# Kernel tuning notes

Hardware: AMD Instinct MI355X
Metric: run time of the kernel (lower is better)

The kernel has to match this reference:

```python
import jax, jax.numpy as jnp
import numpy as np
import math

NUM_HEADS = 16
D_MODEL = 1024
D_HEAD = D_MODEL // NUM_HEADS
B, S = 2, 2048


def setup_inputs() -> dict:
    key = jax.random.key(0)
    k1, k2 = jax.random.split(key)
    query = jax.random.normal(k1, (B, S, D_MODEL), dtype=jnp.float32)
    # causal mask: True where masked (j > i)
    mask = jnp.broadcast_to(jnp.triu(jnp.ones((S, S), dtype=bool), k=1), (B, S, S))
    W_o = jax.random.normal(k2, (D_MODEL, D_MODEL), dtype=jnp.float32) * (1.0 / math.sqrt(D_MODEL))
    b_o = jnp.zeros((D_MODEL,), dtype=jnp.float32)
    return {"query": query, "mask": mask, "W_o": W_o, "b_o": b_o}


def reference(query, mask, W_o, b_o):
    # NOTE: faithful to source — q/k/v linear layers are never applied in forward.
    # Self-attention: key = value = query.
    Bq, Sq, D = query.shape
    # split heads: [B, S, D] -> [B, H, S, dh]
    q = query.reshape(Bq, Sq, NUM_HEADS, D_HEAD).transpose(0, 2, 1, 3)
    k = q
    v = q
    # logits: [B, H, Sq, Sk]
    logits = jnp.einsum("bhqd,bhkd->bhqk", q, k) / math.sqrt(D_HEAD)
    logits = jnp.where(mask[:, None, :, :], -jnp.inf, logits)
    attn = jax.nn.softmax(logits, axis=-1)          # [B, H, Sq, Sk]
    out = jnp.einsum("bhqk,bhkd->bhqd", attn, v)    # [B, H, Sq, dh]
    # merge heads: [B, Sq, D]
    out = out.transpose(0, 2, 1, 3).reshape(Bq, Sq, D)
    # output projection (torch Linear: x @ W.T + b)
    return out @ W_o.T + b_o
```

## Files before the change

kernel.cpp:

```cpp
#include <hip/hip_runtime.h>
#include <hip/hip_bf16.h>
#include <stdint.h>

#define SEQ 2048
#define DMODEL 1024
#define NQT 16

typedef __attribute__((ext_vector_type(8))) short short8;
typedef __attribute__((ext_vector_type(4))) float floatx4;

__device__ __forceinline__ floatx4 mfma16x16x32(short8 a, short8 b, floatx4 c) {
  return __builtin_amdgcn_mfma_f32_16x16x32_bf16(a, b, c, 0, 0, 0);
}

__device__ __forceinline__ uint16_t f2bf(float x) {
  __hip_bfloat16 h = __float2bfloat16(x);
  return *reinterpret_cast<uint16_t*>(&h);
}

__device__ __forceinline__ void glds16(const uint16_t* g, uint16_t* l) {
  __builtin_amdgcn_global_load_lds(
      (const __attribute__((address_space(1))) uint32_t*)g,
      (__attribute__((address_space(3))) uint32_t*)(uint32_t)(uintptr_t)l,
      16, 0, 0);
}

__global__ __launch_bounds__(256) void cvt_kernel(
    const float* __restrict__ src, uint16_t* __restrict__ dst, int n4) {
  int i = blockIdx.x * 256 + threadIdx.x;
  if (i < n4) {
    float4 v = ((const float4*)src)[i];
    ushort4 r;
    r.x = f2bf(v.x); r.y = f2bf(v.y); r.z = f2bf(v.z); r.w = f2bf(v.w);
    ((ushort4*)dst)[i] = r;
  }
}

__device__ __forceinline__ int vt_idx(int d, int key) {
  return d * 64 + ((((key >> 3) ^ (d >> 3)) & 7) << 3) + (key & 7);
}

#define LDPP 72

__global__ __launch_bounds__(256, 2) void attn_kernel(
    const uint16_t* __restrict__ qbf, uint16_t* __restrict__ xout) {
  const int qt   = (NQT - 1) - (blockIdx.x >> 5);
  const int bh   = blockIdx.x & 31;
  const int b    = bh >> 4;
  const int h    = bh & 15;
  const int tid  = threadIdx.x;
  const int wave = tid >> 6;
  const int lane = tid & 63;
  const int l15  = lane & 15;
  const int quad = lane >> 4;

  __shared__ uint16_t Kp[2][2 * 2048];
  __shared__ uint16_t Vt[2][64 * 64];
  __shared__ uint16_t Ps[4][32 * LDPP];

  const uint16_t* kbase = qbf + (size_t)b * SEQ * DMODEL + h * 64;

  short8 qf[2][2];
  #pragma unroll
  for (int s = 0; s < 2; ++s)
    #pragma unroll
    for (int ks = 0; ks < 2; ++ks)
      qf[s][ks] = *(const short8*)(kbase +
          (size_t)(qt * 128 + s * 64 + wave * 16 + l15) * DMODEL + ks * 32 + quad * 8);

  floatx4 o_acc[2][4];
  float l_run[2][4];
  #pragma unroll
  for (int s = 0; s < 2; ++s) {
    #pragma unroll
    for (int dt = 0; dt < 4; ++dt) o_acc[s][dt] = (floatx4){0.f, 0.f, 0.f, 0.f};
    #pragma unroll
    for (int r = 0; r < 4; ++r) l_run[s][r] = 0.f;
  }

  const int r0 = tid >> 3;
  const int cg = (tid & 7) * 8;
  const int gkey = wave * 16 + (lane >> 2);
  const int gkp  = (lane & 3) * 8;

  auto stage = [&](int kt, int buf) {
    uint4 v0 = *(const uint4*)(kbase + (size_t)(kt * 64 + r0) * DMODEL + cg);
    uint4 v1 = *(const uint4*)(kbase + (size_t)(kt * 64 + 32 + r0) * DMODEL + cg);
    glds16(kbase + (size_t)(kt * 64 + gkey) * DMODEL + gkp,
           &Kp[buf][0 * 2048 + wave * 512 + lane * 8]);
    glds16(kbase + (size_t)(kt * 64 + gkey) * DMODEL + 32 + gkp,
           &Kp[buf][1 * 2048 + wave * 512 + lane * 8]);
    uint16_t t0[8], t1[8];
    *(uint4*)t0 = v0;
    *(uint4*)t1 = v1;
    #pragma unroll
    for (int i = 0; i < 8; ++i) Vt[buf][vt_idx(cg + i, r0)] = t0[i];
    #pragma unroll
    for (int i = 0; i < 8; ++i) Vt[buf][vt_idx(cg + i, 32 + r0)] = t1[i];
  };

  const int ktmax = 2 * qt + 1;
  stage(0, 0);

  for (int kt = 0; kt <= ktmax; ++kt) {
    __syncthreads();
    if (kt < ktmax) stage(kt + 1, (kt + 1) & 1);
    const int buf = kt & 1;

    #pragma unroll
    for (int s = 0; s < 2; ++s) {
      if (kt > 2 * qt + s) continue;
      const bool diag = (kt == 2 * qt + s);

      floatx4 sacc[4];
      #pragma unroll
      for (int nt = 0; nt < 4; ++nt) sacc[nt] = (floatx4){0.f, 0.f, 0.f, 0.f};
      #pragma unroll
      for (int ks = 0; ks < 2; ++ks)
        #pragma unroll
        for (int nt = 0; nt < 4; ++nt) {
          short8 kf = *(const short8*)&Kp[buf][ks * 2048 + (nt * 16 + l15) * 32 + quad * 8];
          sacc[nt] = mfma16x16x32(qf[s][ks], kf, sacc[nt]);
        }

      uint16_t* Pw = &Ps[wave][s * 16 * LDPP];
      #pragma unroll
      for (int nt = 0; nt < 4; ++nt) {
        const int lcol = nt * 16 + l15;
        #pragma unroll
        for (int r = 0; r < 4; ++r) {
          float p = __builtin_amdgcn_exp2f(fmaf(sacc[nt][r], 0.1803369f, -10.f));
          if (diag && lcol > wave * 16 + quad * 4 + r) p = 0.f;
          l_run[s][r] += p;
          Pw[(quad * 4 + r) * LDPP + lcol] = f2bf(p);
        }
      }

      #pragma unroll
      for (int ks = 0; ks < 2; ++ks) {
        short8 pf = *(const short8*)&Pw[l15 * LDPP + ks * 32 + quad * 8];
        #pragma unroll
        for (int dt = 0; dt < 4; ++dt) {
          short8 vf = *(const short8*)&Vt[buf][vt_idx(dt * 16 + l15, ks * 32 + quad * 8)];
          o_acc[s][dt] = mfma16x16x32(pf, vf, o_acc[s][dt]);
        }
      }
    }
  }

  #pragma unroll
  for (int s = 0; s < 2; ++s)
    #pragma unroll
    for (int r = 0; r < 4; ++r) {
      float l = l_run[s][r];
      #pragma unroll
      for (int off = 1; off < 16; off <<= 1) l += __shfl_xor(l, off, 64);
      float inv = 1.0f / l;
      int rowg = b * SEQ + qt * 128 + s * 64 + wave * 16 + quad * 4 + r;
      #pragma unroll
      for (int dt = 0; dt < 4; ++dt)
        xout[(size_t)rowg * DMODEL + h * 64 + dt * 16 + l15] =
            f2bf(o_acc[s][dt][r] * inv);
    }
}

__global__ __launch_bounds__(256, 2) void proj_kernel(
    const uint16_t* __restrict__ X, const uint16_t* __restrict__ Wo,
    const float* __restrict__ bo, float* __restrict__ out) {
  const int bx = blockIdx.x;
  const int by = blockIdx.y;
  const int tid = threadIdx.x;
  const int wave = tid >> 6, lane = tid & 63, l15 = lane & 15, quad = lane >> 4;
  const int wr = wave >> 1, wc = wave & 1;

  __shared__ uint16_t As[2][128 * 32];
  __shared__ uint16_t Bs[2][64 * 32];

  floatx4 acc[4][2];
  #pragma unroll
  for (int mt = 0; mt < 4; ++mt)
    #pragma unroll
    for (int nt = 0; nt < 2; ++nt) acc[mt][nt] = (floatx4){0.f, 0.f, 0.f, 0.f};

  const int rA = lane >> 2, kp = (lane & 3) * 8;

  auto stage = [&](int kt, int buf) {
    glds16(X + (size_t)(bx * 128 + wave * 16 + rA) * DMODEL + kt * 32 + kp,
           &As[buf][0 * 2048 + wave * 512 + lane * 8]);
    glds16(X + (size_t)(bx * 128 + 64 + wave * 16 + rA) * DMODEL + kt * 32 + kp,
           &As[buf][1 * 2048 + wave * 512 + lane * 8]);
    glds16(Wo + (size_t)(by * 64 + wave * 16 + rA) * DMODEL + kt * 32 + kp,
           &Bs[buf][wave * 512 + lane * 8]);
  };

  stage(0, 0);
  for (int kt = 0; kt < 32; ++kt) {
    __syncthreads();
    if (kt < 31) stage(kt + 1, (kt + 1) & 1);
    const int buf = kt & 1;
    short8 af[4], bf2[2];
    #pragma unroll
    for (int mt = 0; mt < 4; ++mt)
      af[mt] = *(const short8*)&As[buf][(wr * 64 + mt * 16 + l15) * 32 + quad * 8];
    #pragma unroll
    for (int nt = 0; nt < 2; ++nt)
      bf2[nt] = *(const short8*)&Bs[buf][(wc * 32 + nt * 16 + l15) * 32 + quad * 8];
    #pragma unroll
    for (int mt = 0; mt < 4; ++mt)
      #pragma unroll
      for (int nt = 0; nt < 2; ++nt)
        acc[mt][nt] = mfma16x16x32(af[mt], bf2[nt], acc[mt][nt]);
  }

  #pragma unroll
  for (int nt = 0; nt < 2; ++nt) {
    int colg = by * 64 + wc * 32 + nt * 16 + l15;
    float bias = bo[colg];
    #pragma unroll
    for (int mt = 0; mt < 4; ++mt)
      #pragma unroll
      for (int r2 = 0; r2 < 4; ++r2) {
        int rowg = bx * 128 + wr * 64 + mt * 16 + quad * 4 + r2;
        out[(size_t)rowg * DMODEL + colg] = acc[mt][nt][r2] + bias;
      }
  }
}

extern "C" void kernel_launch(void* const* d_in, const int* in_sizes, int n_in,
                              void* d_out, int out_size, void* d_ws, size_t ws_size,
                              hipStream_t stream) {
  const float* q_f32  = (const float*)d_in[0];
  const float* Wo_f32 = (const float*)d_in[2];
  const float* bo     = (const float*)d_in[3];
  float* out = (float*)d_out;

  uint16_t* qbf  = (uint16_t*)d_ws;
  uint16_t* X    = (uint16_t*)((char*)d_ws + (size_t)8 * 1024 * 1024);
  uint16_t* wobf = (uint16_t*)((char*)d_ws + (size_t)16 * 1024 * 1024);

  const int nq4 = 2 * SEQ * DMODEL / 4;
  const int nw4 = DMODEL * DMODEL / 4;
  cvt_kernel<<<dim3((nq4 + 255) / 256), dim3(256), 0, stream>>>(q_f32, qbf, nq4);
  cvt_kernel<<<dim3((nw4 + 255) / 256), dim3(256), 0, stream>>>(Wo_f32, wobf, nw4);

  attn_kernel<<<dim3(32 * NQT), dim3(256), 0, stream>>>(qbf, X);
  proj_kernel<<<dim3(32, 16), dim3(256), 0, stream>>>(X, wobf, bo, out);
}
```

Before: 170.9 us.

## Shrink attention query tiles, skip masked MFMAs, swizzle LDS, interleave tile order

Each attention block now handles 64 query rows instead of 128, so the grid grows to 1024 blocks, scheduled in an interleaved heavy/light order to balance causal work. K fragments are read straight from global memory rather than staged in LDS. On the diagonal tile, fully masked QK and PV MFMAs are skipped. The P and V tiles get XOR-swizzled LDS layouts, the projection GEMM's LDS loads are swizzled as well, and occupancy hints rise to 4 blocks per CU. The intent is better load balance and parallelism and fewer LDS bank conflicts. In exchange, each block reloads K, the direct global K reads are less coalesced, and register pressure under the higher occupancy hint may cause spills.

```diff
diff --git a/kernel.cpp b/kernel.cpp
--- a/kernel.cpp
+++ b/kernel.cpp
@@ -4,7 +4,6 @@
 
 #define SEQ 2048
 #define DMODEL 1024
-#define NQT 16
 
 typedef __attribute__((ext_vector_type(8))) short short8;
 typedef __attribute__((ext_vector_type(4))) float floatx4;
@@ -37,59 +36,50 @@
 }
 
 __device__ __forceinline__ int vt_idx(int d, int key) {
-  return d * 64 + ((((key >> 3) ^ (d >> 3)) & 7) << 3) + (key & 7);
-}
-
-#define LDPP 72
-
-__global__ __launch_bounds__(256, 2) void attn_kernel(
+  return d * 64 + ((((key >> 3) ^ (d >> 3) ^ d) & 7) << 3) + (key & 7);
+}
+
+__device__ __forceinline__ int ps_idx(int row, int col) {
+  return row * 64 + ((((col >> 3) ^ row) & 7) << 3) + (col & 7);
+}
+
+__global__ __launch_bounds__(256, 4) void attn_kernel(
     const uint16_t* __restrict__ qbf, uint16_t* __restrict__ xout) {
-  const int qt   = (NQT - 1) - (blockIdx.x >> 5);
-  const int bh   = blockIdx.x & 31;
-  const int b    = bh >> 4;
-  const int h    = bh & 15;
+  const int g  = blockIdx.x >> 5;
+  const int qt = (g < 8) ? 31 - g : (g < 16) ? g - 8 : (g < 24) ? 39 - g : g - 16;
+  const int bh = blockIdx.x & 31;
+  const int b  = bh >> 4;
+  const int h  = bh & 15;
   const int tid  = threadIdx.x;
   const int wave = tid >> 6;
   const int lane = tid & 63;
   const int l15  = lane & 15;
   const int quad = lane >> 4;
 
-  __shared__ uint16_t Kp[2][2 * 2048];
   __shared__ uint16_t Vt[2][64 * 64];
-  __shared__ uint16_t Ps[4][32 * LDPP];
-
-  const uint16_t* kbase = qbf + (size_t)b * SEQ * DMODEL + h * 64;
-
-  short8 qf[2][2];
-  #pragma unroll
-  for (int s = 0; s < 2; ++s)
-    #pragma unroll
-    for (int ks = 0; ks < 2; ++ks)
-      qf[s][ks] = *(const short8*)(kbase +
-          (size_t)(qt * 128 + s * 64 + wave * 16 + l15) * DMODEL + ks * 32 + quad * 8);
-
-  floatx4 o_acc[2][4];
-  float l_run[2][4];
-  #pragma unroll
-  for (int s = 0; s < 2; ++s) {
-    #pragma unroll
-    for (int dt = 0; dt < 4; ++dt) o_acc[s][dt] = (floatx4){0.f, 0.f, 0.f, 0.f};
-    #pragma unroll
-    for (int r = 0; r < 4; ++r) l_run[s][r] = 0.f;
-  }
+  __shared__ uint16_t Ps[4][16 * 64];
+
+  const uint16_t* base = qbf + (size_t)b * SEQ * DMODEL + h * 64;
+
+  short8 qf[2];
+  #pragma unroll
+  for (int ks = 0; ks < 2; ++ks)
+    qf[ks] = *(const short8*)(base +
+        (size_t)(qt * 64 + wave * 16 + l15) * DMODEL + ks * 32 + quad * 8);
+
+  floatx4 o_acc[4];
+  float l_run[4];
+  #pragma unroll
+  for (int dt = 0; dt < 4; ++dt) o_acc[dt] = (floatx4){0.f, 0.f, 0.f, 0.f};
+  #pragma unroll
+  for (int r = 0; r < 4; ++r) l_run[r] = 0.f;
 
   const int r0 = tid >> 3;
   const int cg = (tid & 7) * 8;
-  const int gkey = wave * 16 + (lane >> 2);
-  const int gkp  = (lane & 3) * 8;
 
   auto stage = [&](int kt, int buf) {
-    uint4 v0 = *(const uint4*)(kbase + (size_t)(kt * 64 + r0) * DMODEL + cg);
-    uint4 v1 = *(const uint4*)(kbase + (size_t)(kt * 64 + 32 + r0) * DMODEL + cg);
-    glds16(kbase + (size_t)(kt * 64 + gkey) * DMODEL + gkp,
-           &Kp[buf][0 * 2048 + wave * 512 + lane * 8]);
-    glds16(kbase + (size_t)(kt * 64 + gkey) * DMODEL + 32 + gkp,
-           &Kp[buf][1 * 2048 + wave * 512 + lane * 8]);
+    uint4 v0 = *(const uint4*)(base + (size_t)(kt * 64 + r0) * DMODEL + cg);
+    uint4 v1 = *(const uint4*)(base + (size_t)(kt * 64 + 32 + r0) * DMODEL + cg);
     uint16_t t0[8], t1[8];
     *(uint4*)t0 = v0;
     *(uint4*)t1 = v1;
@@ -99,72 +89,75 @@
     for (int i = 0; i < 8; ++i) Vt[buf][vt_idx(cg + i, 32 + r0)] = t1[i];
   };
 
-  const int ktmax = 2 * qt + 1;
   stage(0, 0);
 
-  for (int kt = 0; kt <= ktmax; ++kt) {
+  for (int kt = 0; kt <= qt; ++kt) {
     __syncthreads();
-    if (kt < ktmax) stage(kt + 1, (kt + 1) & 1);
+    if (kt < qt) stage(kt + 1, (kt + 1) & 1);
     const int buf = kt & 1;
-
-    #pragma unroll
-    for (int s = 0; s < 2; ++s) {
-      if (kt > 2 * qt + s) continue;
-      const bool diag = (kt == 2 * qt + s);
-
-      floatx4 sacc[4];
+    const bool diag = (kt == qt);
+    const int ntmax = diag ? wave : 3;
+
+    floatx4 sacc[4];
+    #pragma unroll
+    for (int nt = 0; nt < 4; ++nt) sacc[nt] = (floatx4){0.f, 0.f, 0.f, 0.f};
+    #pragma unroll
+    for (int ks = 0; ks < 2; ++ks)
       #pragma unroll
-      for (int nt = 0; nt < 4; ++nt) sacc[nt] = (floatx4){0.f, 0.f, 0.f, 0.f};
-      #pragma unroll
-      for (int ks = 0; ks < 2; ++ks)
-        #pragma unroll
-        for (int nt = 0; nt < 4; ++nt) {
-          short8 kf = *(const short8*)&Kp[buf][ks * 2048 + (nt * 16 + l15) * 32 + quad * 8];
-          sacc[nt] = mfma16x16x32(qf[s][ks], kf, sacc[nt]);
+      for (int nt = 0; nt < 4; ++nt)
+        if (nt <= ntmax) {
+          short8 kf = *(const short8*)(base +
+              (size_t)(kt * 64 + nt * 16 + l15) * DMODEL + ks * 32 + quad * 8);
+          sacc[nt] = mfma16x16x32(qf[ks], kf, sacc[nt]);
         }
 
-      uint16_t* Pw = &Ps[wave][s * 16 * LDPP];
-      #pragma unroll
-      for (int nt = 0; nt < 4; ++nt) {
-        const int lcol = nt * 16 + l15;
+    uint16_t* Pw = Ps[wave];
+    #pragma unroll
+    for (int nt = 0; nt < 4; ++nt) {
+      const int lcol = nt * 16 + l15;
+      if (nt <= ntmax) {
         #pragma unroll
         for (int r = 0; r < 4; ++r) {
           float p = __builtin_amdgcn_exp2f(fmaf(sacc[nt][r], 0.1803369f, -10.f));
-          if (diag && lcol > wave * 16 + quad * 4 + r) p = 0.f;
-          l_run[s][r] += p;
-          Pw[(quad * 4 + r) * LDPP + lcol] = f2bf(p);
+          if (diag && nt == wave && l15 > quad * 4 + r) p = 0.f;
+          l_run[r] += p;
+          Pw[ps_idx(quad * 4 + r, lcol)] = f2bf(p);
         }
+      } else {
+        #pragma unroll
+        for (int r = 0; r < 4; ++r)
+          Pw[ps_idx(quad * 4 + r, lcol)] = 0;
       }
-
-      #pragma unroll
-      for (int ks = 0; ks < 2; ++ks) {
-        short8 pf = *(const short8*)&Pw[l15 * LDPP + ks * 32 + quad * 8];
+    }
+
+    const int ksmax = (diag && wave < 2) ? 0 : 1;
+    #pragma unroll
+    for (int ks = 0; ks < 2; ++ks)
+      if (ks <= ksmax) {
+        short8 pf = *(const short8*)&Pw[ps_idx(l15, ks * 32 + quad * 8)];
         #pragma unroll
         for (int dt = 0; dt < 4; ++dt) {
           short8 vf = *(const short8*)&Vt[buf][vt_idx(dt * 16 + l15, ks * 32 + quad * 8)];
-          o_acc[s][dt] = mfma16x16x32(pf, vf, o_acc[s][dt]);
+          o_acc[dt] = mfma16x16x32(pf, vf, o_acc[dt]);
         }
       }
-    }
-  }
-
-  #pragma unroll
-  for (int s = 0; s < 2; ++s)
-    #pragma unroll
-    for (int r = 0; r < 4; ++r) {
-      float l = l_run[s][r];
-      #pragma unroll
-      for (int off = 1; off < 16; off <<= 1) l += __shfl_xor(l, off, 64);
-      float inv = 1.0f / l;
-      int rowg = b * SEQ + qt * 128 + s * 64 + wave * 16 + quad * 4 + r;
-      #pragma unroll
-      for (int dt = 0; dt < 4; ++dt)
-        xout[(size_t)rowg * DMODEL + h * 64 + dt * 16 + l15] =
-            f2bf(o_acc[s][dt][r] * inv);
-    }
-}
-
-__global__ __launch_bounds__(256, 2) void proj_kernel(
+  }
+
+  #pragma unroll
+  for (int r = 0; r < 4; ++r) {
+    float l = l_run[r];
+    #pragma unroll
+    for (int off = 1; off < 16; off <<= 1) l += __shfl_xor(l, off, 64);
+    float inv = 1.0f / l;
+    int rowg = b * SEQ + qt * 64 + wave * 16 + quad * 4 + r;
+    #pragma unroll
+    for (int dt = 0; dt < 4; ++dt)
+      xout[(size_t)rowg * DMODEL + h * 64 + dt * 16 + l15] =
+          f2bf(o_acc[dt][r] * inv);
+  }
+}
+
+__global__ __launch_bounds__(256, 4) void proj_kernel(
     const uint16_t* __restrict__ X, const uint16_t* __restrict__ Wo,
     const float* __restrict__ bo, float* __restrict__ out) {
   const int bx = blockIdx.x;
@@ -182,15 +175,16 @@
     #pragma unroll
     for (int nt = 0; nt < 2; ++nt) acc[mt][nt] = (floatx4){0.f, 0.f, 0.f, 0.f};
 
-  const int rA = lane >> 2, kp = (lane & 3) * 8;
+  const int rw = lane >> 2;
+  const int kp = 8 * ((lane & 3) ^ ((lane >> 2) & 3));
 
   auto stage = [&](int kt, int buf) {
-    glds16(X + (size_t)(bx * 128 + wave * 16 + rA) * DMODEL + kt * 32 + kp,
-           &As[buf][0 * 2048 + wave * 512 + lane * 8]);
-    glds16(X + (size_t)(bx * 128 + 64 + wave * 16 + rA) * DMODEL + kt * 32 + kp,
-           &As[buf][1 * 2048 + wave * 512 + lane * 8]);
-    glds16(Wo + (size_t)(by * 64 + wave * 16 + rA) * DMODEL + kt * 32 + kp,
-           &Bs[buf][wave * 512 + lane * 8]);
+    glds16(X + (size_t)(bx * 128 + wave * 16 + rw) * DMODEL + kt * 32 + kp,
+           &As[buf][(wave * 16) * 32 + lane * 8]);
+    glds16(X + (size_t)(bx * 128 + 64 + wave * 16 + rw) * DMODEL + kt * 32 + kp,
+           &As[buf][(64 + wave * 16) * 32 + lane * 8]);
+    glds16(Wo + (size_t)(by * 64 + wave * 16 + rw) * DMODEL + kt * 32 + kp,
+           &Bs[buf][(wave * 16) * 32 + lane * 8]);
   };
 
   stage(0, 0);
@@ -200,11 +194,15 @@
     const int buf = kt & 1;
     short8 af[4], bf2[2];
     #pragma unroll
-    for (int mt = 0; mt < 4; ++mt)
-      af[mt] = *(const short8*)&As[buf][(wr * 64 + mt * 16 + l15) * 32 + quad * 8];
-    #pragma unroll
-    for (int nt = 0; nt < 2; ++nt)
-      bf2[nt] = *(const short8*)&Bs[buf][(wc * 32 + nt * 16 + l15) * 32 + quad * 8];
+    for (int mt = 0; mt < 4; ++mt) {
+      int row = wr * 64 + mt * 16 + l15;
+      af[mt] = *(const short8*)&As[buf][row * 32 + ((quad ^ (row & 3)) << 3)];
+    }
+    #pragma unroll
+    for (int nt = 0; nt < 2; ++nt) {
+      int row = wc * 32 + nt * 16 + l15;
+      bf2[nt] = *(const short8*)&Bs[buf][row * 32 + ((quad ^ (row & 3)) << 3)];
+    }
     #pragma unroll
     for (int mt = 0; mt < 4; ++mt)
       #pragma unroll
@@ -243,6 +241,6 @@
   cvt_kernel<<<dim3((nq4 + 255) / 256), dim3(256), 0, stream>>>(q_f32, qbf, nq4);
   cvt_kernel<<<dim3((nw4 + 255) / 256), dim3(256), 0, stream>>>(Wo_f32, wobf, nw4);
 
-  attn_kernel<<<dim3(32 * NQT), dim3(256), 0, stream>>>(qbf, X);
+  attn_kernel<<<dim3(1024), dim3(256), 0, stream>>>(qbf, X);
   proj_kernel<<<dim3(32, 16), dim3(256), 0, stream>>>(X, wobf, bo, out);
 }
```

Result: slower. 187.9 us (+9.9%).
